# Optimization experiments

Measured on AMD Instinct MI355X. Metric: run time of the kernel, lower is better.

The kernel has to match this reference:

```python
import jax, jax.numpy as jnp
import numpy as np

NEG_INF = -1e30  # stand-in for -inf that is safe under fp16/bf16


def setup_inputs() -> dict:
    key = jax.random.key(0)
    k1, k2, k3, k4, k5 = jax.random.split(key, 5)
    B, NC, H, Wd = 32, 256, 64, 64
    MW, E = 32, 768
    images = jax.random.normal(k1, (B, NC, H, Wd), dtype=jnp.float32)
    words = jax.random.normal(k2, (B, MW, E), dtype=jnp.float32)
    # mask: True where word is ignored; ensure at least one word is attended per row
    mask = jax.random.randint(k3, (B, MW), 0, 2).astype(bool)
    mask = mask.at[:, 0].set(False)
    W = jax.random.normal(k4, (NC, E), dtype=jnp.float32) * (1.0 / np.sqrt(E))
    b = jax.random.normal(k5, (NC,), dtype=jnp.float32) * 0.01
    return {"images": images, "words": words, "mask": mask, "W": W, "b": b}


def reference(images, words, mask, W, b):
    B, NC, H, Wd = images.shape
    _, MW, E = words.shape
    # 1x1 conv over words == linear projection emb_dim -> nc_in
    # words_p: [B, nc_in, max_words]
    words_p = jnp.einsum('bme,ce->bcm', words, W) + b[None, :, None]
    # images flattened to pixels: [B, h*w, nc_in]
    imgs = images.reshape(B, NC, H * Wd).transpose(0, 2, 1)
    # attention scores: [B, h*w, max_words], scaled by 1/sqrt(nc_in)
    attn = jnp.einsum('bpc,bcm->bpm', imgs, words_p) * (1.0 / np.sqrt(NC))
    attn = jnp.where(mask[:, None, :], NEG_INF, attn)
    attn = jax.nn.softmax(attn, axis=-1)
    # weighted word sum per pixel: [B, nc_in, h*w]
    weighted = jnp.einsum('bcm,bpm->bcp', words_p, attn)
    weighted_words = weighted.reshape(B, NC, H, Wd)
    attn_out = attn.transpose(0, 2, 1).reshape(B, MW, H, Wd)
    return weighted_words, attn_out
```

## Files before the change

kernel.cpp:

```cpp
#include <hip/hip_runtime.h>
#include <math.h>

#define B_   32
#define NC_  256
#define HW_  4096
#define MW_  32
#define E_   768
#define NEG_BIG -3.0e38f

#define PART_OFF   0
#define WP_OFF     2097152
#define WT_OFF     2359296
#define WORDST_OFF 2555904
#define MASK_OFF   3342336

__global__ __launch_bounds__(256) void prep_kernel(
    const float* __restrict__ W, const float* __restrict__ words,
    const void* __restrict__ mask_raw,
    float* __restrict__ WT, float* __restrict__ wordsT,
    int* __restrict__ maskn) {
  const int tid = threadIdx.x;
  const int tx = tid & 31, ty = tid >> 5;
  if (blockIdx.x < 192) {
    __shared__ float t[32][33];
    const int tc = blockIdx.x / 24, te = blockIdx.x % 24;
    const int c0 = tc * 32, e0 = te * 32;
#pragma unroll
    for (int k = 0; k < 4; ++k) {
      const int r = ty + 8 * k;
      t[r][tx] = W[(c0 + r) * E_ + e0 + tx];
    }
    __syncthreads();
#pragma unroll
    for (int k = 0; k < 4; ++k) {
      const int r = ty + 8 * k;
      WT[(e0 + r) * NC_ + c0 + tx] = t[tx][r];
    }
  } else if (blockIdx.x < 960) {
    __shared__ float t[32][33];
    const int idx = blockIdx.x - 192;
    const int b = idx / 24, te = idx % 24;
    const int e0 = te * 32;
    const float* wsrc = words + (size_t)b * MW_ * E_;
    float* wdst = wordsT + (size_t)b * E_ * MW_;
#pragma unroll
    for (int k = 0; k < 4; ++k) {
      const int m = ty + 8 * k;
      t[m][tx] = wsrc[m * E_ + e0 + tx];
    }
    __syncthreads();
#pragma unroll
    for (int k = 0; k < 4; ++k) {
      const int e = ty + 8 * k;
      wdst[(e0 + e) * MW_ + tx] = t[tx][e];
    }
  } else {
    __shared__ int is_word;
    if (tid == 0) is_word = 1;
    __syncthreads();
    const int* mi = (const int*)mask_raw;
    const int v = mi[tid];
    if (v != 0 && v != 1 && v != 0x3F800000) is_word = 0;
    __syncthreads();
    if (is_word) {
#pragma unroll
      for (int j = 0; j < 4; ++j) { const int i = j * 256 + tid; maskn[i] = (mi[i] != 0); }
    } else {
      const unsigned char* mb = (const unsigned char*)mask_raw;
#pragma unroll
      for (int j = 0; j < 4; ++j) { const int i = j * 256 + tid; maskn[i] = (mb[i] != 0); }
    }
  }
}

__global__ __launch_bounds__(256) void stage1_partial(
    const float* __restrict__ wordsT, const float* __restrict__ WT,
    float* __restrict__ part) {
  const int c = threadIdx.x;
  const int b = blockIdx.x >> 3;
  const int chunk = blockIdx.x & 7;
  const int e0 = chunk * 96;
  const float* wt = wordsT + (size_t)b * E_ * MW_;
  float acc[32];
#pragma unroll
  for (int m = 0; m < 32; ++m) acc[m] = 0.f;
#pragma unroll 2
  for (int e = e0; e < e0 + 96; ++e) {
    const float wv = WT[(size_t)e * NC_ + c];
    const float* wr = wt + e * MW_;
#pragma unroll
    for (int m = 0; m < 32; ++m) acc[m] = fmaf(wv, wr[m], acc[m]);
  }
  float* pp = part + ((size_t)chunk * 32 + b) * 32 * 256;
#pragma unroll
  for (int m = 0; m < 32; ++m) pp[m * 256 + c] = acc[m];
}

__global__ __launch_bounds__(256) void stage1_reduce(
    const float* __restrict__ part, const float* __restrict__ bias,
    float* __restrict__ wp) {
  const int idx = blockIdx.x * 256 + threadIdx.x;
  const int c = idx & 255;
  const int m = (idx >> 8) & 31;
  const int b = idx >> 13;
  float s = bias[c];
#pragma unroll
  for (int k = 0; k < 8; ++k)
    s += part[(((size_t)k * 32 + b) * 32 + m) * 256 + c];
  wp[((size_t)b * 256 + c) * 32 + m] = s;
}

__global__ __launch_bounds__(256) void attention_main(
    const float* __restrict__ images, const float* __restrict__ wp,
    const int* __restrict__ maskn, float* __restrict__ out_w,
    float* __restrict__ out_a) {
  const int b = blockIdx.x >> 4;
  const int p = ((blockIdx.x & 15) << 8) + threadIdx.x;
  const float* img = images + (size_t)b * NC_ * HW_ + p;
  const float* wpb = wp + (size_t)b * NC_ * MW_;

  float s[32];
#pragma unroll
  for (int m = 0; m < 32; ++m) s[m] = 0.f;

  float cur[16];
#pragma unroll
  for (int j = 0; j < 16; ++j)
    cur[j] = __builtin_nontemporal_load(img + ((size_t)j << 12));

#pragma unroll 1
  for (int c0 = 0; c0 < 256; c0 += 16) {
    float nxt[16];
    if (c0 + 16 < 256) {
#pragma unroll
      for (int j = 0; j < 16; ++j)
        nxt[j] = __builtin_nontemporal_load(img + ((size_t)(c0 + 16 + j) << 12));
    }
#pragma unroll
    for (int j = 0; j < 16; ++j) {
#pragma unroll
      for (int m = 0; m < 32; ++m)
        s[m] = fmaf(cur[j], wpb[((c0 + j) << 5) + m], s[m]);
    }
#pragma unroll
    for (int j = 0; j < 16; ++j) cur[j] = nxt[j];
  }

  unsigned mbits = 0;
#pragma unroll
  for (int m = 0; m < 32; ++m)
    mbits |= (maskn[(b << 5) + m] != 0 ? 1u : 0u) << m;

  float mx = NEG_BIG;
#pragma unroll
  for (int m = 0; m < 32; ++m) {
    s[m] *= 0.0625f;
    if (!((mbits >> m) & 1u)) mx = fmaxf(mx, s[m]);
  }
  float sum = 0.f;
#pragma unroll
  for (int m = 0; m < 32; ++m) {
    const float ev = ((mbits >> m) & 1u) ? 0.f : __expf(s[m] - mx);
    s[m] = ev;
    sum += ev;
  }
  const float inv = 1.f / sum;
#pragma unroll
  for (int m = 0; m < 32; ++m) {
    const float a = s[m] * inv;
    s[m] = a;
    __builtin_nontemporal_store(a, out_a + ((size_t)(b * 32 + m) << 12) + p);
  }

#pragma unroll 1
  for (int c0 = 0; c0 < 256; c0 += 8) {
#pragma unroll
    for (int jc = 0; jc < 8; ++jc) {
      const int c = c0 + jc;
      float o = 0.f;
#pragma unroll
      for (int m = 0; m < 32; ++m)
        o = fmaf(wpb[(c << 5) + m], s[m], o);
      __builtin_nontemporal_store(o, out_w + ((size_t)(b * 256 + c) << 12) + p);
    }
  }
}

extern "C" void kernel_launch(void* const* d_in, const int* in_sizes, int n_in,
                              void* d_out, int out_size, void* d_ws, size_t ws_size,
                              hipStream_t stream) {
  const float* images = (const float*)d_in[0];
  const float* words  = (const float*)d_in[1];
  const void*  mask   = d_in[2];
  const float* W      = (const float*)d_in[3];
  const float* bias   = (const float*)d_in[4];

  float* ws     = (float*)d_ws;
  float* part   = ws + PART_OFF;
  float* wp     = ws + WP_OFF;
  float* WT     = ws + WT_OFF;
  float* wordsT = ws + WORDST_OFF;
  int*   maskn  = (int*)(ws + MASK_OFF);

  float* out_w = (float*)d_out;
  float* out_a = out_w + (size_t)B_ * NC_ * HW_;

  prep_kernel<<<961, 256, 0, stream>>>(W, words, mask, WT, wordsT, maskn);
  stage1_partial<<<256, 256, 0, stream>>>(wordsT, WT, part);
  stage1_reduce<<<1024, 256, 0, stream>>>(part, bias, wp);
  attention_main<<<512, 256, 0, stream>>>(images, wp, maskn, out_w, out_a);
}
```

Baseline: 336.4 us.

## Split channel reduction across four thread groups with shared-memory combine

The attention kernel now uses 512-thread blocks, each covering 128 pixels. Four groups of 128 threads each take 64 channels of the image-by-word-projection dot product, and the partial scores are reduced through shared memory. One group runs the softmax and writes the attention weights to shared memory, then all four groups produce the weighted outputs for their own channel slices. The aim is more parallelism and occupancy, since the old grid had only 512 blocks of 256 threads, each streaming all 256 channels. The cost is extra shared memory, several block barriers, and a softmax phase in which only a quarter of the threads are busy.

New measurement: 545.4 us. +62.1%, slower.

```diff
diff --git a/kernel.cpp b/kernel.cpp
--- a/kernel.cpp
+++ b/kernel.cpp
@@ -110,78 +110,114 @@
   wp[((size_t)b * 256 + c) * 32 + m] = s;
 }
 
-__global__ __launch_bounds__(256) void attention_main(
+__global__ __launch_bounds__(512, 8) void attention_fused(
     const float* __restrict__ images, const float* __restrict__ wp,
     const int* __restrict__ maskn, float* __restrict__ out_w,
     float* __restrict__ out_a) {
-  const int b = blockIdx.x >> 4;
-  const int p = ((blockIdx.x & 15) << 8) + threadIdx.x;
-  const float* img = images + (size_t)b * NC_ * HW_ + p;
+  __shared__ float redA[32][128];
+  __shared__ float redB[32][128];
+  const int t = threadIdx.x;
+  const int px = t & 127;
+  const int g = t >> 7;
+  const int b = blockIdx.x >> 5;
+  const int p = ((blockIdx.x & 31) << 7) + px;
+  const int cbase = g << 6;
+  const float* img = images + ((size_t)b * NC_ + cbase) * HW_ + p;
   const float* wpb = wp + (size_t)b * NC_ * MW_;
 
   float s[32];
 #pragma unroll
   for (int m = 0; m < 32; ++m) s[m] = 0.f;
 
-  float cur[16];
-#pragma unroll
-  for (int j = 0; j < 16; ++j)
+  float cur[8];
+#pragma unroll
+  for (int j = 0; j < 8; ++j)
     cur[j] = __builtin_nontemporal_load(img + ((size_t)j << 12));
 
 #pragma unroll 1
-  for (int c0 = 0; c0 < 256; c0 += 16) {
-    float nxt[16];
-    if (c0 + 16 < 256) {
-#pragma unroll
-      for (int j = 0; j < 16; ++j)
-        nxt[j] = __builtin_nontemporal_load(img + ((size_t)(c0 + 16 + j) << 12));
-    }
-#pragma unroll
-    for (int j = 0; j < 16; ++j) {
+  for (int cc = 0; cc < 64; cc += 8) {
+    float nxt[8];
+    if (cc + 8 < 64) {
+#pragma unroll
+      for (int j = 0; j < 8; ++j)
+        nxt[j] = __builtin_nontemporal_load(img + ((size_t)(cc + 8 + j) << 12));
+    }
+#pragma unroll
+    for (int j = 0; j < 8; ++j) {
+      const int c = cbase + cc + j;
 #pragma unroll
       for (int m = 0; m < 32; ++m)
-        s[m] = fmaf(cur[j], wpb[((c0 + j) << 5) + m], s[m]);
-    }
-#pragma unroll
-    for (int j = 0; j < 16; ++j) cur[j] = nxt[j];
-  }
-
-  unsigned mbits = 0;
-#pragma unroll
-  for (int m = 0; m < 32; ++m)
-    mbits |= (maskn[(b << 5) + m] != 0 ? 1u : 0u) << m;
-
-  float mx = NEG_BIG;
-#pragma unroll
-  for (int m = 0; m < 32; ++m) {
-    s[m] *= 0.0625f;
-    if (!((mbits >> m) & 1u)) mx = fmaxf(mx, s[m]);
-  }
-  float sum = 0.f;
-#pragma unroll
-  for (int m = 0; m < 32; ++m) {
-    const float ev = ((mbits >> m) & 1u) ? 0.f : __expf(s[m] - mx);
-    s[m] = ev;
-    sum += ev;
-  }
-  const float inv = 1.f / sum;
-#pragma unroll
-  for (int m = 0; m < 32; ++m) {
-    const float a = s[m] * inv;
-    s[m] = a;
-    __builtin_nontemporal_store(a, out_a + ((size_t)(b * 32 + m) << 12) + p);
-  }
+        s[m] = fmaf(cur[j], wpb[(c << 5) + m], s[m]);
+    }
+#pragma unroll
+    for (int j = 0; j < 8; ++j) cur[j] = nxt[j];
+  }
+
+  if (g == 2) {
+#pragma unroll
+    for (int m = 0; m < 32; ++m) redA[m][px] = s[m];
+  } else if (g == 3) {
+#pragma unroll
+    for (int m = 0; m < 32; ++m) redB[m][px] = s[m];
+  }
+  __syncthreads();
+  if (g == 0) {
+#pragma unroll
+    for (int m = 0; m < 32; ++m) s[m] += redA[m][px];
+  } else if (g == 1) {
+#pragma unroll
+    for (int m = 0; m < 32; ++m) s[m] += redB[m][px];
+  }
+  __syncthreads();
+  if (g == 1) {
+#pragma unroll
+    for (int m = 0; m < 32; ++m) redA[m][px] = s[m];
+  }
+  __syncthreads();
+
+  if (g == 0) {
+    unsigned mbits = 0;
+#pragma unroll
+    for (int m = 0; m < 32; ++m)
+      mbits |= (maskn[(b << 5) + m] != 0 ? 1u : 0u) << m;
+
+    float mx = NEG_BIG;
+#pragma unroll
+    for (int m = 0; m < 32; ++m) {
+      s[m] = (s[m] + redA[m][px]) * 0.0625f;
+      if (!((mbits >> m) & 1u)) mx = fmaxf(mx, s[m]);
+    }
+    float sum = 0.f;
+#pragma unroll
+    for (int m = 0; m < 32; ++m) {
+      const float ev = ((mbits >> m) & 1u) ? 0.f : __expf(s[m] - mx);
+      s[m] = ev;
+      sum += ev;
+    }
+    const float inv = 1.f / sum;
+#pragma unroll
+    for (int m = 0; m < 32; ++m) {
+      const float a = s[m] * inv;
+      redA[m][px] = a;
+      __builtin_nontemporal_store(a, out_a + ((size_t)((b << 5) + m) << 12) + p);
+    }
+  }
+  __syncthreads();
+
+  float a[32];
+#pragma unroll
+  for (int m = 0; m < 32; ++m) a[m] = redA[m][px];
 
 #pragma unroll 1
-  for (int c0 = 0; c0 < 256; c0 += 8) {
+  for (int cc = 0; cc < 64; cc += 8) {
 #pragma unroll
     for (int jc = 0; jc < 8; ++jc) {
-      const int c = c0 + jc;
+      const int c = cbase + cc + jc;
       float o = 0.f;
 #pragma unroll
       for (int m = 0; m < 32; ++m)
-        o = fmaf(wpb[(c << 5) + m], s[m], o);
-      __builtin_nontemporal_store(o, out_w + ((size_t)(b * 256 + c) << 12) + p);
+        o = fmaf(wpb[(c << 5) + m], a[m], o);
+      __builtin_nontemporal_store(o, out_w + ((size_t)((b << 8) + c) << 12) + p);
     }
   }
 }
@@ -208,5 +244,5 @@
   prep_kernel<<<961, 256, 0, stream>>>(W, words, mask, WT, wordsT, maskn);
   stage1_partial<<<256, 256, 0, stream>>>(wordsT, WT, part);
   stage1_reduce<<<1024, 256, 0, stream>>>(part, bias, wp);
-  attention_main<<<512, 256, 0, stream>>>(images, wp, maskn, out_w, out_a);
-}
+  attention_fused<<<1024, 512, 0, stream>>>(images, wp, maskn, out_w, out_a);
+}
```

## Vectorize pixels per thread and split words across waves in attention kernel

Applied to the files above, without the earlier changes.

The attention kernel now has each thread handle 4 consecutive pixels with float4 loads and stores. The 32 words are split across the 4 waves of a block, so each wave computes 8 scores per pixel. Softmax max and sum are reduced across waves through shared memory, and the full attention vector is shared through LDS for the weighted-sum stage, where each wave produces 64 channels. Mask decoding moves into the attention kernel, which removes the extra prep block and workspace. The aim is wider memory transactions and less redundant wp traffic per pixel, at the cost of extra barriers and higher register pressure.

After: 316.4 us. 1.06x faster.

```diff
diff --git a/kernel.cpp b/kernel.cpp
--- a/kernel.cpp
+++ b/kernel.cpp
@@ -8,17 +8,16 @@
 #define E_   768
 #define NEG_BIG -3.0e38f
 
+typedef float vf4 __attribute__((ext_vector_type(4)));
+
 #define PART_OFF   0
 #define WP_OFF     2097152
 #define WT_OFF     2359296
 #define WORDST_OFF 2555904
-#define MASK_OFF   3342336
 
 __global__ __launch_bounds__(256) void prep_kernel(
     const float* __restrict__ W, const float* __restrict__ words,
-    const void* __restrict__ mask_raw,
-    float* __restrict__ WT, float* __restrict__ wordsT,
-    int* __restrict__ maskn) {
+    float* __restrict__ WT, float* __restrict__ wordsT) {
   const int tid = threadIdx.x;
   const int tx = tid & 31, ty = tid >> 5;
   if (blockIdx.x < 192) {
@@ -36,7 +35,7 @@
       const int r = ty + 8 * k;
       WT[(e0 + r) * NC_ + c0 + tx] = t[tx][r];
     }
-  } else if (blockIdx.x < 960) {
+  } else {
     __shared__ float t[32][33];
     const int idx = blockIdx.x - 192;
     const int b = idx / 24, te = idx % 24;
@@ -53,22 +52,6 @@
     for (int k = 0; k < 4; ++k) {
       const int e = ty + 8 * k;
       wdst[(e0 + e) * MW_ + tx] = t[tx][e];
-    }
-  } else {
-    __shared__ int is_word;
-    if (tid == 0) is_word = 1;
-    __syncthreads();
-    const int* mi = (const int*)mask_raw;
-    const int v = mi[tid];
-    if (v != 0 && v != 1 && v != 0x3F800000) is_word = 0;
-    __syncthreads();
-    if (is_word) {
-#pragma unroll
-      for (int j = 0; j < 4; ++j) { const int i = j * 256 + tid; maskn[i] = (mi[i] != 0); }
-    } else {
-      const unsigned char* mb = (const unsigned char*)mask_raw;
-#pragma unroll
-      for (int j = 0; j < 4; ++j) { const int i = j * 256 + tid; maskn[i] = (mb[i] != 0); }
     }
   }
 }
@@ -110,78 +93,182 @@
   wp[((size_t)b * 256 + c) * 32 + m] = s;
 }
 
-__global__ __launch_bounds__(256) void attention_main(
+__global__ __launch_bounds__(256, 2) void attention_fused(
     const float* __restrict__ images, const float* __restrict__ wp,
-    const int* __restrict__ maskn, float* __restrict__ out_w,
-    float* __restrict__ out_a) {
-  const int b = blockIdx.x >> 4;
-  const int p = ((blockIdx.x & 15) << 8) + threadIdx.x;
-  const float* img = images + (size_t)b * NC_ * HW_ + p;
-  const float* wpb = wp + (size_t)b * NC_ * MW_;
-
-  float s[32];
-#pragma unroll
-  for (int m = 0; m < 32; ++m) s[m] = 0.f;
-
-  float cur[16];
+    const void* __restrict__ mask_raw,
+    float* __restrict__ out_w, float* __restrict__ out_a) {
+  __shared__ vf4 abuf[8][4][64];
+  __shared__ float mxbuf[4][4][64];
+  __shared__ float smbuf[4][4][64];
+  __shared__ int is_word;
+  const int tid = threadIdx.x;
+  const int lane = tid & 63;
+  const int wu = __builtin_amdgcn_readfirstlane(tid >> 6);
+  const int b = blockIdx.x & 31;
+  const int po = ((blockIdx.x >> 5) << 6) + lane;
+  const vf4* imgb = (const vf4*)(images + (size_t)b * NC_ * HW_);
+  const float* wpb = wp + ((size_t)b << 13);
+
+  if (tid == 0) is_word = 1;
+  __syncthreads();
+  {
+    const int* mi = (const int*)mask_raw;
+    const int vv = mi[tid];
+    if (vv != 0 && vv != 1 && vv != 0x3F800000) is_word = 0;
+  }
+  __syncthreads();
+  unsigned mbits = 0;
+  if (is_word) {
+    const int* mi = (const int*)mask_raw;
+#pragma unroll
+    for (int m = 0; m < 32; ++m)
+      mbits |= (mi[(b << 5) + m] != 0 ? 1u : 0u) << m;
+  } else {
+    const unsigned char* mb = (const unsigned char*)mask_raw;
+#pragma unroll
+    for (int m = 0; m < 32; ++m)
+      mbits |= (mb[(b << 5) + m] != 0 ? 1u : 0u) << m;
+  }
+  const unsigned mb8 = (mbits >> (wu << 3)) & 0xFFu;
+
+  float s0[8], s1[8], s2[8], s3[8];
+#pragma unroll
+  for (int m = 0; m < 8; ++m) { s0[m] = 0.f; s1[m] = 0.f; s2[m] = 0.f; s3[m] = 0.f; }
+
+  const float* wps = wpb + (wu << 3);
+
+  vf4 cur[16];
 #pragma unroll
   for (int j = 0; j < 16; ++j)
-    cur[j] = __builtin_nontemporal_load(img + ((size_t)j << 12));
+    cur[j] = __builtin_nontemporal_load(&imgb[((size_t)j << 10) + po]);
 
 #pragma unroll 1
   for (int c0 = 0; c0 < 256; c0 += 16) {
-    float nxt[16];
+    vf4 nxt[16];
     if (c0 + 16 < 256) {
 #pragma unroll
       for (int j = 0; j < 16; ++j)
-        nxt[j] = __builtin_nontemporal_load(img + ((size_t)(c0 + 16 + j) << 12));
+        nxt[j] = __builtin_nontemporal_load(&imgb[((size_t)(c0 + 16 + j) << 10) + po]);
     }
 #pragma unroll
     for (int j = 0; j < 16; ++j) {
-#pragma unroll
-      for (int m = 0; m < 32; ++m)
-        s[m] = fmaf(cur[j], wpb[((c0 + j) << 5) + m], s[m]);
+      const float* wr = wps + ((c0 + j) << 5);
+      const vf4 v = cur[j];
+#pragma unroll
+      for (int m = 0; m < 8; ++m) {
+        s0[m] = fmaf(v.x, wr[m], s0[m]);
+        s1[m] = fmaf(v.y, wr[m], s1[m]);
+        s2[m] = fmaf(v.z, wr[m], s2[m]);
+        s3[m] = fmaf(v.w, wr[m], s3[m]);
+      }
     }
 #pragma unroll
     for (int j = 0; j < 16; ++j) cur[j] = nxt[j];
   }
 
-  unsigned mbits = 0;
-#pragma unroll
-  for (int m = 0; m < 32; ++m)
-    mbits |= (maskn[(b << 5) + m] != 0 ? 1u : 0u) << m;
-
-  float mx = NEG_BIG;
-#pragma unroll
-  for (int m = 0; m < 32; ++m) {
-    s[m] *= 0.0625f;
-    if (!((mbits >> m) & 1u)) mx = fmaxf(mx, s[m]);
-  }
-  float sum = 0.f;
-#pragma unroll
-  for (int m = 0; m < 32; ++m) {
-    const float ev = ((mbits >> m) & 1u) ? 0.f : __expf(s[m] - mx);
-    s[m] = ev;
-    sum += ev;
-  }
-  const float inv = 1.f / sum;
-#pragma unroll
-  for (int m = 0; m < 32; ++m) {
-    const float a = s[m] * inv;
-    s[m] = a;
-    __builtin_nontemporal_store(a, out_a + ((size_t)(b * 32 + m) << 12) + p);
-  }
-
+  float l0 = NEG_BIG, l1 = NEG_BIG, l2 = NEG_BIG, l3 = NEG_BIG;
+#pragma unroll
+  for (int m = 0; m < 8; ++m) {
+    s0[m] *= 0.0625f; s1[m] *= 0.0625f; s2[m] *= 0.0625f; s3[m] *= 0.0625f;
+    if (!((mb8 >> m) & 1u)) {
+      l0 = fmaxf(l0, s0[m]); l1 = fmaxf(l1, s1[m]);
+      l2 = fmaxf(l2, s2[m]); l3 = fmaxf(l3, s3[m]);
+    }
+  }
+  mxbuf[wu][0][lane] = l0; mxbuf[wu][1][lane] = l1;
+  mxbuf[wu][2][lane] = l2; mxbuf[wu][3][lane] = l3;
+  __syncthreads();
+  float g0 = mxbuf[0][0][lane], g1 = mxbuf[0][1][lane];
+  float g2 = mxbuf[0][2][lane], g3 = mxbuf[0][3][lane];
+#pragma unroll
+  for (int w2 = 1; w2 < 4; ++w2) {
+    g0 = fmaxf(g0, mxbuf[w2][0][lane]); g1 = fmaxf(g1, mxbuf[w2][1][lane]);
+    g2 = fmaxf(g2, mxbuf[w2][2][lane]); g3 = fmaxf(g3, mxbuf[w2][3][lane]);
+  }
+  float t0 = 0.f, t1 = 0.f, t2 = 0.f, t3 = 0.f;
+#pragma unroll
+  for (int m = 0; m < 8; ++m) {
+    const bool msk = (mb8 >> m) & 1u;
+    const float e0 = msk ? 0.f : __expf(s0[m] - g0);
+    const float e1 = msk ? 0.f : __expf(s1[m] - g1);
+    const float e2 = msk ? 0.f : __expf(s2[m] - g2);
+    const float e3 = msk ? 0.f : __expf(s3[m] - g3);
+    s0[m] = e0; s1[m] = e1; s2[m] = e2; s3[m] = e3;
+    t0 += e0; t1 += e1; t2 += e2; t3 += e3;
+  }
+  smbuf[wu][0][lane] = t0; smbuf[wu][1][lane] = t1;
+  smbuf[wu][2][lane] = t2; smbuf[wu][3][lane] = t3;
+  __syncthreads();
+  float u0 = smbuf[0][0][lane], u1 = smbuf[0][1][lane];
+  float u2 = smbuf[0][2][lane], u3 = smbuf[0][3][lane];
+#pragma unroll
+  for (int w2 = 1; w2 < 4; ++w2) {
+    u0 += smbuf[w2][0][lane]; u1 += smbuf[w2][1][lane];
+    u2 += smbuf[w2][2][lane]; u3 += smbuf[w2][3][lane];
+  }
+  const float i0 = 1.f / u0, i1 = 1.f / u1, i2 = 1.f / u2, i3 = 1.f / u3;
+#pragma unroll
+  for (int m = 0; m < 8; ++m) {
+    s0[m] *= i0; s1[m] *= i1; s2[m] *= i2; s3[m] *= i3;
+  }
+
+  {
+    vf4* oa = (vf4*)out_a;
+#pragma unroll
+    for (int m = 0; m < 8; ++m) {
+      vf4 a; a.x = s0[m]; a.y = s1[m]; a.z = s2[m]; a.w = s3[m];
+      __builtin_nontemporal_store(
+          a, &oa[(((size_t)(b << 5) + (wu << 3) + m) << 10) + po]);
+    }
+  }
+
+  {
+    vf4 q0, q1;
+    q0.x = s0[0]; q0.y = s0[1]; q0.z = s0[2]; q0.w = s0[3];
+    q1.x = s0[4]; q1.y = s0[5]; q1.z = s0[6]; q1.w = s0[7];
+    abuf[(wu << 1)][0][lane] = q0; abuf[(wu << 1) + 1][0][lane] = q1;
+    q0.x = s1[0]; q0.y = s1[1]; q0.z = s1[2]; q0.w = s1[3];
+    q1.x = s1[4]; q1.y = s1[5]; q1.z = s1[6]; q1.w = s1[7];
+    abuf[(wu << 1)][1][lane] = q0; abuf[(wu << 1) + 1][1][lane] = q1;
+    q0.x = s2[0]; q0.y = s2[1]; q0.z = s2[2]; q0.w = s2[3];
+    q1.x = s2[4]; q1.y = s2[5]; q1.z = s2[6]; q1.w = s2[7];
+    abuf[(wu << 1)][2][lane] = q0; abuf[(wu << 1) + 1][2][lane] = q1;
+    q0.x = s3[0]; q0.y = s3[1]; q0.z = s3[2]; q0.w = s3[3];
+    q1.x = s3[4]; q1.y = s3[5]; q1.z = s3[6]; q1.w = s3[7];
+    abuf[(wu << 1)][3][lane] = q0; abuf[(wu << 1) + 1][3][lane] = q1;
+  }
+  __syncthreads();
+
+  float a0[32], a1[32], a2[32], a3[32];
+#pragma unroll
+  for (int mq = 0; mq < 8; ++mq) {
+    const vf4 x0 = abuf[mq][0][lane];
+    a0[4 * mq] = x0.x; a0[4 * mq + 1] = x0.y; a0[4 * mq + 2] = x0.z; a0[4 * mq + 3] = x0.w;
+    const vf4 x1 = abuf[mq][1][lane];
+    a1[4 * mq] = x1.x; a1[4 * mq + 1] = x1.y; a1[4 * mq + 2] = x1.z; a1[4 * mq + 3] = x1.w;
+    const vf4 x2 = abuf[mq][2][lane];
+    a2[4 * mq] = x2.x; a2[4 * mq + 1] = x2.y; a2[4 * mq + 2] = x2.z; a2[4 * mq + 3] = x2.w;
+    const vf4 x3 = abuf[mq][3][lane];
+    a3[4 * mq] = x3.x; a3[4 * mq + 1] = x3.y; a3[4 * mq + 2] = x3.z; a3[4 * mq + 3] = x3.w;
+  }
+
+  vf4* ow = (vf4*)out_w;
 #pragma unroll 1
-  for (int c0 = 0; c0 < 256; c0 += 8) {
-#pragma unroll
-    for (int jc = 0; jc < 8; ++jc) {
-      const int c = c0 + jc;
-      float o = 0.f;
-#pragma unroll
-      for (int m = 0; m < 32; ++m)
-        o = fmaf(wpb[(c << 5) + m], s[m], o);
-      __builtin_nontemporal_store(o, out_w + ((size_t)(b * 256 + c) << 12) + p);
+  for (int c0 = 0; c0 < 64; c0 += 4) {
+#pragma unroll
+    for (int j = 0; j < 4; ++j) {
+      const int c = (wu << 6) + c0 + j;
+      const float* wr = wpb + (c << 5);
+      float o0 = 0.f, o1 = 0.f, o2 = 0.f, o3 = 0.f;
+#pragma unroll
+      for (int m = 0; m < 32; ++m) {
+        o0 = fmaf(wr[m], a0[m], o0);
+        o1 = fmaf(wr[m], a1[m], o1);
+        o2 = fmaf(wr[m], a2[m], o2);
+        o3 = fmaf(wr[m], a3[m], o3);
+      }
+      vf4 o; o.x = o0; o.y = o1; o.z = o2; o.w = o3;
+      __builtin_nontemporal_store(o, &ow[(((size_t)(b << 8) + c) << 10) + po]);
     }
   }
 }
@@ -200,13 +287,12 @@
   float* wp     = ws + WP_OFF;
   float* WT     = ws + WT_OFF;
   float* wordsT = ws + WORDST_OFF;
-  int*   maskn  = (int*)(ws + MASK_OFF);
 
   float* out_w = (float*)d_out;
   float* out_a = out_w + (size_t)B_ * NC_ * HW_;
 
-  prep_kernel<<<961, 256, 0, stream>>>(W, words, mask, WT, wordsT, maskn);
+  prep_kernel<<<960, 256, 0, stream>>>(W, words, WT, wordsT);
   stage1_partial<<<256, 256, 0, stream>>>(wordsT, WT, part);
   stage1_reduce<<<1024, 256, 0, stream>>>(part, bias, wp);
-  attention_main<<<512, 256, 0, stream>>>(images, wp, maskn, out_w, out_a);
-}
+  attention_fused<<<512, 256, 0, stream>>>(images, wp, mask, out_w, out_a);
+}
```
